# Kernel optimization log

Measured on AMD Instinct MI355X. Metric: run time of the kernel, lower is better.

## Reference

```python
import jax, jax.numpy as jnp
import numpy as np

N_NODE = 50000
N_EDGE = 800000
D = 64       # in_dim = out_dim = hidden_dim
A = 64       # attn_dim
N_REL = 475  # 2*237+1 relation ids
B = 32       # batch of queries


def setup_inputs() -> dict:
    key = jax.random.key(0)
    ks = jax.random.split(key, 16)
    hidden = jax.random.normal(ks[0], (N_NODE, D), dtype=jnp.float32)
    sub = jax.random.randint(ks[1], (N_EDGE,), 0, N_NODE)
    rel = jax.random.randint(ks[2], (N_EDGE,), 0, N_REL)
    obj = jax.random.randint(ks[3], (N_EDGE,), 0, N_NODE)
    edges = jnp.stack([sub, rel, obj], axis=1)  # [E, 3]
    gnn_emb_rel = jax.random.normal(ks[4], (N_REL, D), dtype=jnp.float32)
    mapping = jax.random.randint(ks[5], (N_REL,), 0, N_REL)  # rel id -> unique-rel row
    q_rel = jax.random.randint(ks[6], (B,), 0, N_REL)
    r_idx = jax.random.randint(ks[7], (N_EDGE,), 0, B)  # edge -> query index
    s = 1.0 / np.sqrt(D)
    sa = 1.0 / np.sqrt(A)
    u = lambda k, shape, b: jax.random.uniform(k, shape, jnp.float32, minval=-b, maxval=b)
    return {
        "hidden": hidden,
        "edges": edges,
        "gnn_emb_rel": gnn_emb_rel,
        "mapping": mapping,
        "q_rel": q_rel,
        "r_idx": r_idx,
        "n_node": N_NODE,
        "Ws_w": u(ks[8], (A, D), s),
        "Wr_w": u(ks[9], (A, D), s),
        "Wqr_w": u(ks[10], (A, D), s),
        "Wqr_b": u(ks[11], (A,), s),
        "walpha_w": u(ks[12], (1, A), sa),
        "walpha_b": u(ks[13], (1,), sa),
        "Wh_w": u(ks[14], (D, D), s),
    }


def reference(hidden, edges, gnn_emb_rel, mapping, q_rel, r_idx, n_node,
              Ws_w, Wr_w, Wqr_w, Wqr_b, walpha_w, walpha_b, Wh_w):
    sub, rel, obj = edges[:, 0], edges[:, 1], edges[:, 2]
    hs = hidden[sub]                       # [E, D] gather
    hr = gnn_emb_rel[mapping[rel]]         # [E, D] gather
    # per-query h_qr projected once, then gathered per edge (same math, cheaper)
    hq = gnn_emb_rel[mapping[q_rel]]       # [B, D]
    qr_attn = hq @ Wqr_w.T + Wqr_b         # [B, A]
    pre = hs @ Ws_w.T + hr @ Wr_w.T + qr_attn[r_idx]   # [E, A]
    alpha = jax.nn.sigmoid(jax.nn.relu(pre) @ walpha_w.T + walpha_b)  # [E, 1]
    message = alpha * (hs * hr)            # [E, D]
    message_agg = jax.ops.segment_sum(message, obj, num_segments=n_node)  # [N, D]
    hidden_new = jax.nn.relu(message_agg @ Wh_w.T)  # act = ReLU from GNN_auto
    return hidden_new
```

## Files before the change

kernel.cpp:

```cpp
#include <hip/hip_runtime.h>
#include <hip/hip_bf16.h>

#define D64 64
#define LPAD 68

typedef __attribute__((ext_vector_type(8))) short short8;
typedef __attribute__((ext_vector_type(4))) float f32x4;

__device__ inline float lane_bcast(float v, int l) {
    return __uint_as_float(__builtin_amdgcn_readlane(__float_as_uint(v), l));
}
__device__ inline float bf16_lo(unsigned u) { return __uint_as_float(u << 16); }
__device__ inline float bf16_hi(unsigned u) { return __uint_as_float(u & 0xFFFF0000u); }
__device__ inline float bf16u(unsigned short u) { return __uint_as_float((unsigned)u << 16); }
__device__ inline unsigned short f2bf(float f) {
    __hip_bfloat16 b = __float2bfloat16(f);
    return *(unsigned short*)&b;
}

__global__ void prep_kernel(const float* __restrict__ emb, const int* __restrict__ mapping,
                            const int* __restrict__ q_rel,
                            const float* __restrict__ Wr, const float* __restrict__ Wqr,
                            const float* __restrict__ Wqr_b, const float* __restrict__ Ws,
                            const float* __restrict__ Wh,
                            unsigned short* __restrict__ hrmapb,
                            unsigned short* __restrict__ hrWb,
                            unsigned short* __restrict__ qrb,
                            unsigned short* __restrict__ WsB,
                            unsigned short* __restrict__ WhB,
                            int* __restrict__ counts, int nrel, int nq, int NN) {
    int b = blockIdx.x;
    int lane = threadIdx.x;
    if (b < nrel) {
        int m = mapping[b];
        float v = emb[m * D64 + lane];
        hrmapb[b * D64 + lane] = f2bf(v);
        float acc = 0.f;
#pragma unroll
        for (int d = 0; d < D64; ++d)
            acc = fmaf(lane_bcast(v, d), Wr[lane * D64 + d], acc);
        hrWb[b * D64 + lane] = f2bf(acc);
    } else if (b < nrel + nq) {
        int q = b - nrel;
        int m = mapping[q_rel[q]];
        float v = emb[m * D64 + lane];
        float acc = Wqr_b[lane];
#pragma unroll
        for (int d = 0; d < D64; ++d)
            acc = fmaf(lane_bcast(v, d), Wqr[lane * D64 + d], acc);
        qrb[q * D64 + lane] = f2bf(acc);
    } else if (b < nrel + nq + 64) {
        int c = b - nrel - nq;
        WsB[c * D64 + lane] = f2bf(Ws[c * D64 + lane]);
    } else if (b < nrel + nq + 128) {
        int c = b - nrel - nq - 64;
        WhB[c * D64 + lane] = f2bf(Wh[c * D64 + lane]);
    } else {
        int c = b - nrel - nq - 128;
        int idx = c * 64 + lane;
        if (idx < NN) counts[idx] = 0;
    }
}

__global__ void comb_kernel(const unsigned short* __restrict__ hrWb,
                            const unsigned short* __restrict__ qrb,
                            unsigned short* __restrict__ combb, int nrel) {
    int i = blockIdx.x * blockDim.x + threadIdx.x;
    int total = nrel * 32 * D64;
    if (i < total) {
        int lane = i & 63;
        int row = i >> 6;
        int r = row >> 5;
        int q = row & 31;
        combb[i] = f2bf(bf16u(hrWb[r * D64 + lane]) + bf16u(qrb[q * D64 + lane]));
    }
}

__global__ void __launch_bounds__(64)
rowmm_mfma_kernel(const float* __restrict__ in,
                  const unsigned short* __restrict__ WsB,
                  unsigned short* __restrict__ outb,
                  unsigned short* __restrict__ inb, int nrows,
                  const int* __restrict__ edges, const int* __restrict__ r_idx,
                  int* __restrict__ counts, uint2* __restrict__ epack, int E) {
    __shared__ unsigned short la[16 * LPAD];
    int lane = threadIdx.x;
    int rbase = blockIdx.x * 16;

    if (rbase < nrows) {
        short8 bfrag[8];
#pragma unroll
        for (int t = 0; t < 4; ++t)
#pragma unroll
            for (int kk = 0; kk < 2; ++kk)
                bfrag[t * 2 + kk] = *(const short8*)(WsB + (size_t)(t * 16 + (lane & 15)) * D64 +
                                                     kk * 32 + (lane >> 4) * 8);

        bool full = (rbase + 16 <= nrows);
        float v[16];
        if (full) {
#pragma unroll
            for (int rr = 0; rr < 16; ++rr)
                v[rr] = in[(size_t)(rbase + rr) * D64 + lane];
        } else {
#pragma unroll
            for (int rr = 0; rr < 16; ++rr)
                v[rr] = (rbase + rr < nrows) ? in[(size_t)(rbase + rr) * D64 + lane] : 0.f;
        }
#pragma unroll
        for (int rr = 0; rr < 16; ++rr) {
            unsigned short bb = f2bf(v[rr]);
            if (rbase + rr < nrows) inb[(size_t)(rbase + rr) * D64 + lane] = bb;
            la[rr * LPAD + lane] = bb;
        }

        f32x4 acc[4];
#pragma unroll
        for (int t = 0; t < 4; ++t) acc[t] = (f32x4){0.f, 0.f, 0.f, 0.f};
#pragma unroll
        for (int kk = 0; kk < 2; ++kk) {
            short8 afrag = *(const short8*)(la + (lane & 15) * LPAD + kk * 32 + (lane >> 4) * 8);
#pragma unroll
            for (int t = 0; t < 4; ++t)
                acc[t] = __builtin_amdgcn_mfma_f32_16x16x32_bf16(afrag, bfrag[t * 2 + kk],
                                                                 acc[t], 0, 0, 0);
        }
#pragma unroll
        for (int t = 0; t < 4; ++t)
#pragma unroll
            for (int reg = 0; reg < 4; ++reg) {
                int row = rbase + (lane >> 4) * 4 + reg;
                int col = t * 16 + (lane & 15);
                if (row < nrows)
                    outb[(size_t)row * D64 + col] = f2bf(acc[t][reg]);
            }
    }

    int n4 = E >> 2;
    const uint4* e4 = (const uint4*)edges;
    for (int i4 = blockIdx.x * 64 + lane; i4 < n4; i4 += gridDim.x * 64) {
        uint4 a = e4[i4 * 3 + 0];
        uint4 b = e4[i4 * 3 + 1];
        uint4 c = e4[i4 * 3 + 2];
        uint4 r = ((const uint4*)r_idx)[i4];
        uint4 p01 = make_uint4(a.x | ((((a.y << 5) | r.x)) << 17), a.z,
                               a.w | ((((b.x << 5) | r.y)) << 17), b.y);
        uint4 p23 = make_uint4(b.z | ((((b.w << 5) | r.z)) << 17), c.x,
                               c.y | ((((c.z << 5) | r.w)) << 17), c.w);
        ((uint4*)epack)[i4 * 2 + 0] = p01;
        ((uint4*)epack)[i4 * 2 + 1] = p23;
        atomicAdd(&counts[a.z], 1);
        atomicAdd(&counts[b.y], 1);
        atomicAdd(&counts[c.x], 1);
        atomicAdd(&counts[c.w], 1);
    }
    int tail = n4 * 4;
    int gt = blockIdx.x * 64 + lane;
    int ti = tail + gt;
    if (gt < (E - tail) && ti < E) {
        unsigned sub = edges[ti * 3 + 0];
        unsigned rel = edges[ti * 3 + 1];
        unsigned obj = edges[ti * 3 + 2];
        unsigned ri  = r_idx[ti];
        epack[ti] = make_uint2(sub | (((rel << 5) | ri) << 17), obj);
        atomicAdd(&counts[obj], 1);
    }
}

__global__ void scan1_kernel(const int* __restrict__ counts, int* __restrict__ offs,
                             int* __restrict__ partials, int n) {
    __shared__ int tsum[256];
    int t = threadIdx.x;
    int base = blockIdx.x * 1024 + t * 4;
    int v[4];
    int s = 0;
#pragma unroll
    for (int i = 0; i < 4; ++i) {
        int idx = base + i;
        int c = (idx < n) ? counts[idx] : 0;
        v[i] = s;
        s += c;
    }
    tsum[t] = s;
    __syncthreads();
    for (int off = 1; off < 256; off <<= 1) {
        int y = (t >= off) ? tsum[t - off] : 0;
        __syncthreads();
        tsum[t] += y;
        __syncthreads();
    }
    int incl = tsum[t];
    int thread_prefix = incl - s;
    if (t == 255) partials[blockIdx.x] = incl;
#pragma unroll
    for (int i = 0; i < 4; ++i) {
        int idx = base + i;
        if (idx < n) offs[idx] = thread_prefix + v[i];
    }
}

__global__ void scan2_kernel(int* partials, int nb) {
    int t = threadIdx.x;
    int own = (t < nb) ? partials[t] : 0;
    int v = own;
    for (int off = 1; off < 64; off <<= 1) {
        int y = __shfl_up(v, off, 64);
        if (t >= off) v += y;
    }
    if (t < nb) partials[t] = v - own;
}

__global__ void scan3_kernel(int* __restrict__ offs, const int* __restrict__ partials, int n) {
    int base = blockIdx.x * 1024 + threadIdx.x;
    int add = partials[blockIdx.x];
#pragma unroll
    for (int i = 0; i < 4; ++i) {
        int idx = base + i * 256;
        if (idx < n) offs[idx] += add;
    }
}

__global__ void alpha_scatter_kernel(const uint2* __restrict__ epack,
                                     const unsigned short* __restrict__ hsWb,
                                     const unsigned short* __restrict__ combb,
                                     const float* __restrict__ walpha_w,
                                     const float* __restrict__ walpha_b,
                                     int* __restrict__ offs, int2* __restrict__ rec,
                                     int E, int half) {
    int tid = blockIdx.x * blockDim.x + threadIdx.x;
    int e0 = tid >> 3;
    int l = tid & 7;
    if (e0 >= half) return;
    int e1 = e0 + half;
    bool has1 = (e1 < E);

    uint2 p0 = epack[e0];
    uint2 p1 = has1 ? epack[e1] : make_uint2(0u, 0u);
    unsigned sub0 = p0.x & 0x1FFFF, comb0 = p0.x >> 17;
    unsigned sub1 = p1.x & 0x1FFFF, comb1 = p1.x >> 17;
    int obj0 = (int)p0.y, obj1 = (int)p1.y;

    uint4 hv0 = *(const uint4*)(hsWb  + (size_t)sub0  * D64 + l * 8);
    uint4 cv0 = *(const uint4*)(combb + (size_t)comb0 * D64 + l * 8);
    uint4 hv1 = *(const uint4*)(hsWb  + (size_t)sub1  * D64 + l * 8);
    uint4 cv1 = *(const uint4*)(combb + (size_t)comb1 * D64 + l * 8);
    const float4* w = (const float4*)(walpha_w + l * 8);
    float4 w0 = w[0], w1 = w[1];

    float x0, x1;
    x0 = fmaxf(bf16_lo(hv0.x) + bf16_lo(cv0.x), 0.f) * w0.x;
    x0 = fmaf(fmaxf(bf16_hi(hv0.x) + bf16_hi(cv0.x), 0.f), w0.y, x0);
    x0 = fmaf(fmaxf(bf16_lo(hv0.y) + bf16_lo(cv0.y), 0.f), w0.z, x0);
    x0 = fmaf(fmaxf(bf16_hi(hv0.y) + bf16_hi(cv0.y), 0.f), w0.w, x0);
    x0 = fmaf(fmaxf(bf16_lo(hv0.z) + bf16_lo(cv0.z), 0.f), w1.x, x0);
    x0 = fmaf(fmaxf(bf16_hi(hv0.z) + bf16_hi(cv0.z), 0.f), w1.y, x0);
    x0 = fmaf(fmaxf(bf16_lo(hv0.w) + bf16_lo(cv0.w), 0.f), w1.z, x0);
    x0 = fmaf(fmaxf(bf16_hi(hv0.w) + bf16_hi(cv0.w), 0.f), w1.w, x0);

    x1 = fmaxf(bf16_lo(hv1.x) + bf16_lo(cv1.x), 0.f) * w0.x;
    x1 = fmaf(fmaxf(bf16_hi(hv1.x) + bf16_hi(cv1.x), 0.f), w0.y, x1);
    x1 = fmaf(fmaxf(bf16_lo(hv1.y) + bf16_lo(cv1.y), 0.f), w0.z, x1);
    x1 = fmaf(fmaxf(bf16_hi(hv1.y) + bf16_hi(cv1.y), 0.f), w0.w, x1);
    x1 = fmaf(fmaxf(bf16_lo(hv1.z) + bf16_lo(cv1.z), 0.f), w1.x, x1);
    x1 = fmaf(fmaxf(bf16_hi(hv1.z) + bf16_hi(cv1.z), 0.f), w1.y, x1);
    x1 = fmaf(fmaxf(bf16_lo(hv1.w) + bf16_lo(cv1.w), 0.f), w1.z, x1);
    x1 = fmaf(fmaxf(bf16_hi(hv1.w) + bf16_hi(cv1.w), 0.f), w1.w, x1);

    x0 += __shfl_xor(x0, 4, 64);
    x1 += __shfl_xor(x1, 4, 64);
    x0 += __shfl_xor(x0, 2, 64);
    x1 += __shfl_xor(x1, 2, 64);
    x0 += __shfl_xor(x0, 1, 64);
    x1 += __shfl_xor(x1, 1, 64);

    if (l == 0) {
        float wb = walpha_b[0];
        float a0 = 1.f / (1.f + __expf(-(x0 + wb)));
        int rel0 = comb0 >> 5;
        int slot0 = atomicAdd(&offs[obj0], 1);
        rec[slot0] = make_int2((int)(sub0 | (rel0 << 17)), __float_as_int(a0));
        if (has1) {
            float a1 = 1.f / (1.f + __expf(-(x1 + wb)));
            int rel1 = comb1 >> 5;
            int slot1 = atomicAdd(&offs[obj1], 1);
            rec[slot1] = make_int2((int)(sub1 | (rel1 << 17)), __float_as_int(a1));
        }
    }
}

__global__ void agg_kernel(const int2* __restrict__ rec, const int* __restrict__ endoff,
                           const unsigned short* __restrict__ hiddenb,
                           const unsigned short* __restrict__ hrmapb,
                           unsigned short* __restrict__ aggb, int NN) {
    int tid = threadIdx.x;
    int lane = tid & 63;
    int n = (blockIdx.x * blockDim.x + tid) >> 6;
    if (n >= NN) return;
    int start = (n == 0) ? 0 : endoff[n - 1];
    int end = endoff[n];
    start = __builtin_amdgcn_readfirstlane(start);
    end = __builtin_amdgcn_readfirstlane(end);
    float acc0 = 0.f, acc1 = 0.f, acc2 = 0.f, acc3 = 0.f;
    for (int base = start; base < end; base += 64) {
        int cnt = end - base;
        if (cnt > 64) cnt = 64;
        int rx = 0, ry = 0;
        if (lane < cnt) {
            int2 r = rec[base + lane];
            rx = r.x; ry = r.y;
        }
        int j = 0;
        for (; j + 7 < cnt; j += 8) {
            int a_rx[8], a_ry[8];
#pragma unroll
            for (int k = 0; k < 8; ++k) {
                a_rx[k] = __builtin_amdgcn_readlane(rx, j + k);
                a_ry[k] = __builtin_amdgcn_readlane(ry, j + k);
            }
            float h[8], m[8];
#pragma unroll
            for (int k = 0; k < 8; ++k) {
                h[k] = bf16u(hiddenb[(size_t)(a_rx[k] & 0x1FFFF) * D64 + lane]);
                m[k] = bf16u(hrmapb[(size_t)((unsigned)a_rx[k] >> 17) * D64 + lane]);
            }
            acc0 = fmaf(__uint_as_float(a_ry[0]) * h[0], m[0], acc0);
            acc1 = fmaf(__uint_as_float(a_ry[1]) * h[1], m[1], acc1);
            acc2 = fmaf(__uint_as_float(a_ry[2]) * h[2], m[2], acc2);
            acc3 = fmaf(__uint_as_float(a_ry[3]) * h[3], m[3], acc3);
            acc0 = fmaf(__uint_as_float(a_ry[4]) * h[4], m[4], acc0);
            acc1 = fmaf(__uint_as_float(a_ry[5]) * h[5], m[5], acc1);
            acc2 = fmaf(__uint_as_float(a_ry[6]) * h[6], m[6], acc2);
            acc3 = fmaf(__uint_as_float(a_ry[7]) * h[7], m[7], acc3);
        }
        for (; j + 3 < cnt; j += 4) {
            int rx0 = __builtin_amdgcn_readlane(rx, j);
            int ry0 = __builtin_amdgcn_readlane(ry, j);
            int rx1 = __builtin_amdgcn_readlane(rx, j + 1);
            int ry1 = __builtin_amdgcn_readlane(ry, j + 1);
            int rx2 = __builtin_amdgcn_readlane(rx, j + 2);
            int ry2 = __builtin_amdgcn_readlane(ry, j + 2);
            int rx3 = __builtin_amdgcn_readlane(rx, j + 3);
            int ry3 = __builtin_amdgcn_readlane(ry, j + 3);
            float h0 = bf16u(hiddenb[(size_t)(rx0 & 0x1FFFF) * D64 + lane]);
            float m0 = bf16u(hrmapb[(size_t)((unsigned)rx0 >> 17) * D64 + lane]);
            float h1 = bf16u(hiddenb[(size_t)(rx1 & 0x1FFFF) * D64 + lane]);
            float m1 = bf16u(hrmapb[(size_t)((unsigned)rx1 >> 17) * D64 + lane]);
            float h2 = bf16u(hiddenb[(size_t)(rx2 & 0x1FFFF) * D64 + lane]);
            float m2 = bf16u(hrmapb[(size_t)((unsigned)rx2 >> 17) * D64 + lane]);
            float h3 = bf16u(hiddenb[(size_t)(rx3 & 0x1FFFF) * D64 + lane]);
            float m3 = bf16u(hrmapb[(size_t)((unsigned)rx3 >> 17) * D64 + lane]);
            acc0 = fmaf(__uint_as_float(ry0) * h0, m0, acc0);
            acc1 = fmaf(__uint_as_float(ry1) * h1, m1, acc1);
            acc2 = fmaf(__uint_as_float(ry2) * h2, m2, acc2);
            acc3 = fmaf(__uint_as_float(ry3) * h3, m3, acc3);
        }
        for (; j < cnt; ++j) {
            int rx0 = __builtin_amdgcn_readlane(rx, j);
            int ry0 = __builtin_amdgcn_readlane(ry, j);
            float h0 = bf16u(hiddenb[(size_t)(rx0 & 0x1FFFF) * D64 + lane]);
            float m0 = bf16u(hrmapb[(size_t)((unsigned)rx0 >> 17) * D64 + lane]);
            acc0 = fmaf(__uint_as_float(ry0) * h0, m0, acc0);
        }
    }
    aggb[(size_t)n * D64 + lane] = f2bf((acc0 + acc1) + (acc2 + acc3));
}

__global__ void rowmm_wh_kernel(const unsigned short* __restrict__ aggb,
                                const unsigned short* __restrict__ WhB,
                                float* __restrict__ out, int nrows) {
    int lane = threadIdx.x;
    int rbase = blockIdx.x * 16;
    if (rbase >= nrows) return;

    short8 bfrag[8];
#pragma unroll
    for (int t = 0; t < 4; ++t)
#pragma unroll
        for (int kk = 0; kk < 2; ++kk)
            bfrag[t * 2 + kk] = *(const short8*)(WhB + (size_t)(t * 16 + (lane & 15)) * D64 +
                                                 kk * 32 + (lane >> 4) * 8);

    f32x4 acc[4];
#pragma unroll
    for (int t = 0; t < 4; ++t) acc[t] = (f32x4){0.f, 0.f, 0.f, 0.f};
#pragma unroll
    for (int kk = 0; kk < 2; ++kk) {
        short8 afrag = *(const short8*)(aggb + (size_t)(rbase + (lane & 15)) * D64 +
                                        kk * 32 + (lane >> 4) * 8);
#pragma unroll
        for (int t = 0; t < 4; ++t)
            acc[t] = __builtin_amdgcn_mfma_f32_16x16x32_bf16(afrag, bfrag[t * 2 + kk],
                                                             acc[t], 0, 0, 0);
    }
#pragma unroll
    for (int t = 0; t < 4; ++t)
#pragma unroll
        for (int reg = 0; reg < 4; ++reg) {
            int row = rbase + (lane >> 4) * 4 + reg;
            int col = t * 16 + (lane & 15);
            if (row < nrows)
                out[(size_t)row * D64 + col] = fmaxf(acc[t][reg], 0.f);
        }
}

extern "C" void kernel_launch(void* const* d_in, const int* in_sizes, int n_in,
                              void* d_out, int out_size, void* d_ws, size_t ws_size,
                              hipStream_t stream) {
    const float* hidden   = (const float*)d_in[0];
    const int*   edges    = (const int*)d_in[1];
    const float* emb_rel  = (const float*)d_in[2];
    const int*   mapping  = (const int*)d_in[3];
    const int*   q_rel    = (const int*)d_in[4];
    const int*   r_idx    = (const int*)d_in[5];
    const float* Ws_w     = (const float*)d_in[7];
    const float* Wr_w     = (const float*)d_in[8];
    const float* Wqr_w    = (const float*)d_in[9];
    const float* Wqr_b    = (const float*)d_in[10];
    const float* walpha_w = (const float*)d_in[11];
    const float* walpha_b = (const float*)d_in[12];
    const float* Wh_w     = (const float*)d_in[13];
    float* out = (float*)d_out;

    int NN   = in_sizes[0] / D64;
    int E    = in_sizes[5];
    int NREL = in_sizes[3];
    int NQ   = in_sizes[4];

    char* ws = (char*)d_ws;
    size_t off = 0;
    unsigned short* hsWb    = (unsigned short*)(ws + off); off += (size_t)NN * D64 * 2;
    unsigned short* hiddenb = (unsigned short*)(ws + off); off += (size_t)NN * D64 * 2;
    int2*  rec  = (int2*)(ws + off);       off += (size_t)E * sizeof(int2);
    uint2* epack = (uint2*)(ws + off);     off += (size_t)E * sizeof(uint2);
    unsigned short* aggb = (unsigned short*)epack;
    int* counts = (int*)(ws + off);        off += (size_t)NN * sizeof(int);
    int* offs   = (int*)(ws + off);        off += (size_t)NN * sizeof(int);
    int* partials = (int*)(ws + off);      off += 64 * sizeof(int);
    unsigned short* hrmapb = (unsigned short*)(ws + off); off += (size_t)NREL * D64 * 2;
    unsigned short* hrWb   = (unsigned short*)(ws + off); off += (size_t)NREL * D64 * 2;
    unsigned short* qrb    = (unsigned short*)(ws + off); off += (size_t)NQ * D64 * 2;
    unsigned short* WsB    = (unsigned short*)(ws + off); off += (size_t)D64 * D64 * 2;
    unsigned short* WhB    = (unsigned short*)(ws + off); off += (size_t)D64 * D64 * 2;
    unsigned short* combb  = (unsigned short*)(ws + off); off += (size_t)NREL * 32 * D64 * 2;

    int NB = (NN + 1023) / 1024;
    int zblocks = (NN + 63) / 64;

    prep_kernel<<<NREL + NQ + 128 + zblocks, 64, 0, stream>>>(
        emb_rel, mapping, q_rel, Wr_w, Wqr_w, Wqr_b, Ws_w, Wh_w,
        hrmapb, hrWb, qrb, WsB, WhB, counts, NREL, NQ, NN);
    comb_kernel<<<(NREL * 32 * D64 + 255) / 256, 256, 0, stream>>>(hrWb, qrb, combb, NREL);
    rowmm_mfma_kernel<<<(NN + 15) / 16, 64, 0, stream>>>(hidden, WsB, hsWb, hiddenb, NN,
                                                         edges, r_idx, counts, epack, E);
    scan1_kernel<<<NB, 256, 0, stream>>>(counts, offs, partials, NN);
    scan2_kernel<<<1, 64, 0, stream>>>(partials, NB);
    scan3_kernel<<<NB, 256, 0, stream>>>(offs, partials, NN);
    {
        int half = (E + 1) / 2;
        long long threads = (long long)half * 8;
        int blocks = (int)((threads + 255) / 256);
        alpha_scatter_kernel<<<blocks, 256, 0, stream>>>(epack, hsWb, combb,
                                                         walpha_w, walpha_b, offs, rec, E, half);
    }
    agg_kernel<<<(NN * 64 + 1023) / 1024, 1024, 0, stream>>>(rec, offs, hiddenb, hrmapb,
                                                             aggb, NN);
    rowmm_wh_kernel<<<(NN + 15) / 16, 64, 0, stream>>>(aggb, WhB, out, NN);
}
```

Measured before the change: 139.8 us.

## Fuse attention computation into CSR aggregation and interleave projected/raw node features

Attention scoring moves out of the separate edge-parallel alpha_scatter kernel and into the per-node aggregation kernel, which recomputes alpha with a full 64-lane wave reduction for each edge. The projected features hs·Ws and the raw bf16 hidden values are stored interleaved as one 32-bit pair, so a single gather supplies both. The scatter step now writes a packed 4-byte record built straight from edges, which removes the intermediate epack buffer and the 8-byte alpha records. In exchange, aggregation does a 6-step shuffle reduction per edge and gathers from combb per lane, which adds serial work inside the node loop.

```diff
diff --git a/kernel.cpp b/kernel.cpp
--- a/kernel.cpp
+++ b/kernel.cpp
@@ -79,10 +79,9 @@
 __global__ void __launch_bounds__(64)
 rowmm_mfma_kernel(const float* __restrict__ in,
                   const unsigned short* __restrict__ WsB,
-                  unsigned short* __restrict__ outb,
-                  unsigned short* __restrict__ inb, int nrows,
-                  const int* __restrict__ edges, const int* __restrict__ r_idx,
-                  int* __restrict__ counts, uint2* __restrict__ epack, int E) {
+                  unsigned* __restrict__ pairb, int nrows,
+                  const int* __restrict__ edges,
+                  int* __restrict__ counts, int E) {
     __shared__ unsigned short la[16 * LPAD];
     int lane = threadIdx.x;
     int rbase = blockIdx.x * 16;
@@ -108,11 +107,8 @@
                 v[rr] = (rbase + rr < nrows) ? in[(size_t)(rbase + rr) * D64 + lane] : 0.f;
         }
 #pragma unroll
-        for (int rr = 0; rr < 16; ++rr) {
-            unsigned short bb = f2bf(v[rr]);
-            if (rbase + rr < nrows) inb[(size_t)(rbase + rr) * D64 + lane] = bb;
-            la[rr * LPAD + lane] = bb;
-        }
+        for (int rr = 0; rr < 16; ++rr)
+            la[rr * LPAD + lane] = f2bf(v[rr]);
 
         f32x4 acc[4];
 #pragma unroll
@@ -129,10 +125,14 @@
         for (int t = 0; t < 4; ++t)
 #pragma unroll
             for (int reg = 0; reg < 4; ++reg) {
-                int row = rbase + (lane >> 4) * 4 + reg;
+                int rl = (lane >> 4) * 4 + reg;
                 int col = t * 16 + (lane & 15);
-                if (row < nrows)
-                    outb[(size_t)row * D64 + col] = f2bf(acc[t][reg]);
+                int row = rbase + rl;
+                if (row < nrows) {
+                    unsigned hid = la[rl * LPAD + col];
+                    unsigned pr = (unsigned)f2bf(acc[t][reg]) | (hid << 16);
+                    pairb[(size_t)row * D64 + col] = pr;
+                }
             }
     }
 
@@ -142,13 +142,6 @@
         uint4 a = e4[i4 * 3 + 0];
         uint4 b = e4[i4 * 3 + 1];
         uint4 c = e4[i4 * 3 + 2];
-        uint4 r = ((const uint4*)r_idx)[i4];
-        uint4 p01 = make_uint4(a.x | ((((a.y << 5) | r.x)) << 17), a.z,
-                               a.w | ((((b.x << 5) | r.y)) << 17), b.y);
-        uint4 p23 = make_uint4(b.z | ((((b.w << 5) | r.z)) << 17), c.x,
-                               c.y | ((((c.z << 5) | r.w)) << 17), c.w);
-        ((uint4*)epack)[i4 * 2 + 0] = p01;
-        ((uint4*)epack)[i4 * 2 + 1] = p23;
         atomicAdd(&counts[a.z], 1);
         atomicAdd(&counts[b.y], 1);
         atomicAdd(&counts[c.x], 1);
@@ -157,14 +150,8 @@
     int tail = n4 * 4;
     int gt = blockIdx.x * 64 + lane;
     int ti = tail + gt;
-    if (gt < (E - tail) && ti < E) {
-        unsigned sub = edges[ti * 3 + 0];
-        unsigned rel = edges[ti * 3 + 1];
-        unsigned obj = edges[ti * 3 + 2];
-        unsigned ri  = r_idx[ti];
-        epack[ti] = make_uint2(sub | (((rel << 5) | ri) << 17), obj);
-        atomicAdd(&counts[obj], 1);
-    }
+    if (gt < (E - tail) && ti < E)
+        atomicAdd(&counts[edges[ti * 3 + 2]], 1);
 }
 
 __global__ void scan1_kernel(const int* __restrict__ counts, int* __restrict__ offs,
@@ -220,149 +207,109 @@
     }
 }
 
-__global__ void alpha_scatter_kernel(const uint2* __restrict__ epack,
-                                     const unsigned short* __restrict__ hsWb,
-                                     const unsigned short* __restrict__ combb,
-                                     const float* __restrict__ walpha_w,
-                                     const float* __restrict__ walpha_b,
-                                     int* __restrict__ offs, int2* __restrict__ rec,
-                                     int E, int half) {
-    int tid = blockIdx.x * blockDim.x + threadIdx.x;
-    int e0 = tid >> 3;
-    int l = tid & 7;
-    if (e0 >= half) return;
-    int e1 = e0 + half;
-    bool has1 = (e1 < E);
-
-    uint2 p0 = epack[e0];
-    uint2 p1 = has1 ? epack[e1] : make_uint2(0u, 0u);
-    unsigned sub0 = p0.x & 0x1FFFF, comb0 = p0.x >> 17;
-    unsigned sub1 = p1.x & 0x1FFFF, comb1 = p1.x >> 17;
-    int obj0 = (int)p0.y, obj1 = (int)p1.y;
-
-    uint4 hv0 = *(const uint4*)(hsWb  + (size_t)sub0  * D64 + l * 8);
-    uint4 cv0 = *(const uint4*)(combb + (size_t)comb0 * D64 + l * 8);
-    uint4 hv1 = *(const uint4*)(hsWb  + (size_t)sub1  * D64 + l * 8);
-    uint4 cv1 = *(const uint4*)(combb + (size_t)comb1 * D64 + l * 8);
-    const float4* w = (const float4*)(walpha_w + l * 8);
-    float4 w0 = w[0], w1 = w[1];
-
-    float x0, x1;
-    x0 = fmaxf(bf16_lo(hv0.x) + bf16_lo(cv0.x), 0.f) * w0.x;
-    x0 = fmaf(fmaxf(bf16_hi(hv0.x) + bf16_hi(cv0.x), 0.f), w0.y, x0);
-    x0 = fmaf(fmaxf(bf16_lo(hv0.y) + bf16_lo(cv0.y), 0.f), w0.z, x0);
-    x0 = fmaf(fmaxf(bf16_hi(hv0.y) + bf16_hi(cv0.y), 0.f), w0.w, x0);
-    x0 = fmaf(fmaxf(bf16_lo(hv0.z) + bf16_lo(cv0.z), 0.f), w1.x, x0);
-    x0 = fmaf(fmaxf(bf16_hi(hv0.z) + bf16_hi(cv0.z), 0.f), w1.y, x0);
-    x0 = fmaf(fmaxf(bf16_lo(hv0.w) + bf16_lo(cv0.w), 0.f), w1.z, x0);
-    x0 = fmaf(fmaxf(bf16_hi(hv0.w) + bf16_hi(cv0.w), 0.f), w1.w, x0);
-
-    x1 = fmaxf(bf16_lo(hv1.x) + bf16_lo(cv1.x), 0.f) * w0.x;
-    x1 = fmaf(fmaxf(bf16_hi(hv1.x) + bf16_hi(cv1.x), 0.f), w0.y, x1);
-    x1 = fmaf(fmaxf(bf16_lo(hv1.y) + bf16_lo(cv1.y), 0.f), w0.z, x1);
-    x1 = fmaf(fmaxf(bf16_hi(hv1.y) + bf16_hi(cv1.y), 0.f), w0.w, x1);
-    x1 = fmaf(fmaxf(bf16_lo(hv1.z) + bf16_lo(cv1.z), 0.f), w1.x, x1);
-    x1 = fmaf(fmaxf(bf16_hi(hv1.z) + bf16_hi(cv1.z), 0.f), w1.y, x1);
-    x1 = fmaf(fmaxf(bf16_lo(hv1.w) + bf16_lo(cv1.w), 0.f), w1.z, x1);
-    x1 = fmaf(fmaxf(bf16_hi(hv1.w) + bf16_hi(cv1.w), 0.f), w1.w, x1);
-
-    x0 += __shfl_xor(x0, 4, 64);
-    x1 += __shfl_xor(x1, 4, 64);
-    x0 += __shfl_xor(x0, 2, 64);
-    x1 += __shfl_xor(x1, 2, 64);
-    x0 += __shfl_xor(x0, 1, 64);
-    x1 += __shfl_xor(x1, 1, 64);
-
-    if (l == 0) {
-        float wb = walpha_b[0];
-        float a0 = 1.f / (1.f + __expf(-(x0 + wb)));
-        int rel0 = comb0 >> 5;
-        int slot0 = atomicAdd(&offs[obj0], 1);
-        rec[slot0] = make_int2((int)(sub0 | (rel0 << 17)), __float_as_int(a0));
-        if (has1) {
-            float a1 = 1.f / (1.f + __expf(-(x1 + wb)));
-            int rel1 = comb1 >> 5;
-            int slot1 = atomicAdd(&offs[obj1], 1);
-            rec[slot1] = make_int2((int)(sub1 | (rel1 << 17)), __float_as_int(a1));
-        }
-    }
-}
-
-__global__ void agg_kernel(const int2* __restrict__ rec, const int* __restrict__ endoff,
-                           const unsigned short* __restrict__ hiddenb,
+__global__ void scatter_kernel(const int* __restrict__ edges, const int* __restrict__ r_idx,
+                               int* __restrict__ offs, unsigned* __restrict__ rec, int E) {
+    int i4 = blockIdx.x * blockDim.x + threadIdx.x;
+    int n4 = E >> 2;
+    if (i4 < n4) {
+        const uint4* e4 = (const uint4*)edges;
+        uint4 a = e4[i4 * 3 + 0];
+        uint4 b = e4[i4 * 3 + 1];
+        uint4 c = e4[i4 * 3 + 2];
+        uint4 r = ((const uint4*)r_idx)[i4];
+        int s0 = atomicAdd(&offs[a.z], 1);
+        rec[s0] = a.x | ((((a.y << 5) | r.x)) << 17);
+        int s1 = atomicAdd(&offs[b.y], 1);
+        rec[s1] = a.w | ((((b.x << 5) | r.y)) << 17);
+        int s2 = atomicAdd(&offs[c.x], 1);
+        rec[s2] = b.z | ((((b.w << 5) | r.z)) << 17);
+        int s3 = atomicAdd(&offs[c.w], 1);
+        rec[s3] = c.y | ((((c.z << 5) | r.w)) << 17);
+    }
+    int tail = n4 * 4;
+    int ti = tail + i4;
+    if (i4 < (E - tail) && ti < E) {
+        unsigned sub = edges[ti * 3 + 0];
+        unsigned rel = edges[ti * 3 + 1];
+        unsigned obj = edges[ti * 3 + 2];
+        unsigned ri  = r_idx[ti];
+        int s = atomicAdd(&offs[(int)obj], 1);
+        rec[s] = sub | (((rel << 5) | ri) << 17);
+    }
+}
+
+__global__ void agg_kernel(const unsigned* __restrict__ rec, const int* __restrict__ endoff,
+                           const unsigned* __restrict__ pairb,
+                           const unsigned short* __restrict__ combb,
                            const unsigned short* __restrict__ hrmapb,
+                           const float* __restrict__ walpha_w,
+                           const float* __restrict__ walpha_b,
                            unsigned short* __restrict__ aggb, int NN) {
     int tid = threadIdx.x;
     int lane = tid & 63;
     int n = (blockIdx.x * blockDim.x + tid) >> 6;
     if (n >= NN) return;
+    float wa = walpha_w[lane];
+    float wb = walpha_b[0];
     int start = (n == 0) ? 0 : endoff[n - 1];
     int end = endoff[n];
     start = __builtin_amdgcn_readfirstlane(start);
     end = __builtin_amdgcn_readfirstlane(end);
-    float acc0 = 0.f, acc1 = 0.f, acc2 = 0.f, acc3 = 0.f;
+    float acc0 = 0.f, acc1 = 0.f;
     for (int base = start; base < end; base += 64) {
         int cnt = end - base;
         if (cnt > 64) cnt = 64;
-        int rx = 0, ry = 0;
-        if (lane < cnt) {
-            int2 r = rec[base + lane];
-            rx = r.x; ry = r.y;
+        unsigned rv = 0;
+        if (lane < cnt) rv = rec[base + lane];
+        int j = 0;
+        for (; j + 1 < cnt; j += 2) {
+            unsigned r0 = (unsigned)__builtin_amdgcn_readlane((int)rv, j);
+            unsigned r1 = (unsigned)__builtin_amdgcn_readlane((int)rv, j + 1);
+            unsigned sub0 = r0 & 0x1FFFF, cb0 = r0 >> 17;
+            unsigned sub1 = r1 & 0x1FFFF, cb1 = r1 >> 17;
+            unsigned pv0 = pairb[(size_t)sub0 * D64 + lane];
+            unsigned cv0 = (unsigned)combb[(size_t)cb0 * D64 + lane];
+            unsigned mv0 = (unsigned)hrmapb[(size_t)(cb0 >> 5) * D64 + lane];
+            unsigned pv1 = pairb[(size_t)sub1 * D64 + lane];
+            unsigned cv1 = (unsigned)combb[(size_t)cb1 * D64 + lane];
+            unsigned mv1 = (unsigned)hrmapb[(size_t)(cb1 >> 5) * D64 + lane];
+            float x0 = fmaxf(bf16_lo(pv0) + __uint_as_float(cv0 << 16), 0.f) * wa;
+            float x1 = fmaxf(bf16_lo(pv1) + __uint_as_float(cv1 << 16), 0.f) * wa;
+            x0 += __shfl_xor(x0, 32, 64);
+            x1 += __shfl_xor(x1, 32, 64);
+            x0 += __shfl_xor(x0, 16, 64);
+            x1 += __shfl_xor(x1, 16, 64);
+            x0 += __shfl_xor(x0, 8, 64);
+            x1 += __shfl_xor(x1, 8, 64);
+            x0 += __shfl_xor(x0, 4, 64);
+            x1 += __shfl_xor(x1, 4, 64);
+            x0 += __shfl_xor(x0, 2, 64);
+            x1 += __shfl_xor(x1, 2, 64);
+            x0 += __shfl_xor(x0, 1, 64);
+            x1 += __shfl_xor(x1, 1, 64);
+            float al0 = 1.f / (1.f + __expf(-(x0 + wb)));
+            float al1 = 1.f / (1.f + __expf(-(x1 + wb)));
+            acc0 = fmaf(al0 * bf16_hi(pv0), __uint_as_float(mv0 << 16), acc0);
+            acc1 = fmaf(al1 * bf16_hi(pv1), __uint_as_float(mv1 << 16), acc1);
         }
-        int j = 0;
-        for (; j + 7 < cnt; j += 8) {
-            int a_rx[8], a_ry[8];
-#pragma unroll
-            for (int k = 0; k < 8; ++k) {
-                a_rx[k] = __builtin_amdgcn_readlane(rx, j + k);
-                a_ry[k] = __builtin_amdgcn_readlane(ry, j + k);
-            }
-            float h[8], m[8];
-#pragma unroll
-            for (int k = 0; k < 8; ++k) {
-                h[k] = bf16u(hiddenb[(size_t)(a_rx[k] & 0x1FFFF) * D64 + lane]);
-                m[k] = bf16u(hrmapb[(size_t)((unsigned)a_rx[k] >> 17) * D64 + lane]);
-            }
-            acc0 = fmaf(__uint_as_float(a_ry[0]) * h[0], m[0], acc0);
-            acc1 = fmaf(__uint_as_float(a_ry[1]) * h[1], m[1], acc1);
-            acc2 = fmaf(__uint_as_float(a_ry[2]) * h[2], m[2], acc2);
-            acc3 = fmaf(__uint_as_float(a_ry[3]) * h[3], m[3], acc3);
-            acc0 = fmaf(__uint_as_float(a_ry[4]) * h[4], m[4], acc0);
-            acc1 = fmaf(__uint_as_float(a_ry[5]) * h[5], m[5], acc1);
-            acc2 = fmaf(__uint_as_float(a_ry[6]) * h[6], m[6], acc2);
-            acc3 = fmaf(__uint_as_float(a_ry[7]) * h[7], m[7], acc3);
+        if (j < cnt) {
+            unsigned r0 = (unsigned)__builtin_amdgcn_readlane((int)rv, j);
+            unsigned sub0 = r0 & 0x1FFFF, cb0 = r0 >> 17;
+            unsigned pv0 = pairb[(size_t)sub0 * D64 + lane];
+            unsigned cv0 = (unsigned)combb[(size_t)cb0 * D64 + lane];
+            unsigned mv0 = (unsigned)hrmapb[(size_t)(cb0 >> 5) * D64 + lane];
+            float x0 = fmaxf(bf16_lo(pv0) + __uint_as_float(cv0 << 16), 0.f) * wa;
+            x0 += __shfl_xor(x0, 32, 64);
+            x0 += __shfl_xor(x0, 16, 64);
+            x0 += __shfl_xor(x0, 8, 64);
+            x0 += __shfl_xor(x0, 4, 64);
+            x0 += __shfl_xor(x0, 2, 64);
+            x0 += __shfl_xor(x0, 1, 64);
+            float al0 = 1.f / (1.f + __expf(-(x0 + wb)));
+            acc0 = fmaf(al0 * bf16_hi(pv0), __uint_as_float(mv0 << 16), acc0);
         }
-        for (; j + 3 < cnt; j += 4) {
-            int rx0 = __builtin_amdgcn_readlane(rx, j);
-            int ry0 = __builtin_amdgcn_readlane(ry, j);
-            int rx1 = __builtin_amdgcn_readlane(rx, j + 1);
-            int ry1 = __builtin_amdgcn_readlane(ry, j + 1);
-            int rx2 = __builtin_amdgcn_readlane(rx, j + 2);
-            int ry2 = __builtin_amdgcn_readlane(ry, j + 2);
-            int rx3 = __builtin_amdgcn_readlane(rx, j + 3);
-            int ry3 = __builtin_amdgcn_readlane(ry, j + 3);
-            float h0 = bf16u(hiddenb[(size_t)(rx0 & 0x1FFFF) * D64 + lane]);
-            float m0 = bf16u(hrmapb[(size_t)((unsigned)rx0 >> 17) * D64 + lane]);
-            float h1 = bf16u(hiddenb[(size_t)(rx1 & 0x1FFFF) * D64 + lane]);
-            float m1 = bf16u(hrmapb[(size_t)((unsigned)rx1 >> 17) * D64 + lane]);
-            float h2 = bf16u(hiddenb[(size_t)(rx2 & 0x1FFFF) * D64 + lane]);
-            float m2 = bf16u(hrmapb[(size_t)((unsigned)rx2 >> 17) * D64 + lane]);
-            float h3 = bf16u(hiddenb[(size_t)(rx3 & 0x1FFFF) * D64 + lane]);
-            float m3 = bf16u(hrmapb[(size_t)((unsigned)rx3 >> 17) * D64 + lane]);
-            acc0 = fmaf(__uint_as_float(ry0) * h0, m0, acc0);
-            acc1 = fmaf(__uint_as_float(ry1) * h1, m1, acc1);
-            acc2 = fmaf(__uint_as_float(ry2) * h2, m2, acc2);
-            acc3 = fmaf(__uint_as_float(ry3) * h3, m3, acc3);
-        }
-        for (; j < cnt; ++j) {
-            int rx0 = __builtin_amdgcn_readlane(rx, j);
-            int ry0 = __builtin_amdgcn_readlane(ry, j);
-            float h0 = bf16u(hiddenb[(size_t)(rx0 & 0x1FFFF) * D64 + lane]);
-            float m0 = bf16u(hrmapb[(size_t)((unsigned)rx0 >> 17) * D64 + lane]);
-            acc0 = fmaf(__uint_as_float(ry0) * h0, m0, acc0);
-        }
-    }
-    aggb[(size_t)n * D64 + lane] = f2bf((acc0 + acc1) + (acc2 + acc3));
+    }
+    aggb[(size_t)n * D64 + lane] = f2bf(acc0 + acc1);
 }
 
 __global__ void rowmm_wh_kernel(const unsigned short* __restrict__ aggb,
@@ -428,11 +375,9 @@
 
     char* ws = (char*)d_ws;
     size_t off = 0;
-    unsigned short* hsWb    = (unsigned short*)(ws + off); off += (size_t)NN * D64 * 2;
-    unsigned short* hiddenb = (unsigned short*)(ws + off); off += (size_t)NN * D64 * 2;
-    int2*  rec  = (int2*)(ws + off);       off += (size_t)E * sizeof(int2);
-    uint2* epack = (uint2*)(ws + off);     off += (size_t)E * sizeof(uint2);
-    unsigned short* aggb = (unsigned short*)epack;
+    unsigned* pairb  = (unsigned*)(ws + off);       off += (size_t)NN * D64 * 4;
+    unsigned short* aggb = (unsigned short*)(ws + off); off += (size_t)NN * D64 * 2;
+    unsigned* rec    = (unsigned*)(ws + off);       off += (size_t)E * 4;
     int* counts = (int*)(ws + off);        off += (size_t)NN * sizeof(int);
     int* offs   = (int*)(ws + off);        off += (size_t)NN * sizeof(int);
     int* partials = (int*)(ws + off);      off += 64 * sizeof(int);
@@ -450,19 +395,16 @@
         emb_rel, mapping, q_rel, Wr_w, Wqr_w, Wqr_b, Ws_w, Wh_w,
         hrmapb, hrWb, qrb, WsB, WhB, counts, NREL, NQ, NN);
     comb_kernel<<<(NREL * 32 * D64 + 255) / 256, 256, 0, stream>>>(hrWb, qrb, combb, NREL);
-    rowmm_mfma_kernel<<<(NN + 15) / 16, 64, 0, stream>>>(hidden, WsB, hsWb, hiddenb, NN,
-                                                         edges, r_idx, counts, epack, E);
+    rowmm_mfma_kernel<<<(NN + 15) / 16, 64, 0, stream>>>(hidden, WsB, pairb, NN,
+                                                         edges, counts, E);
     scan1_kernel<<<NB, 256, 0, stream>>>(counts, offs, partials, NN);
     scan2_kernel<<<1, 64, 0, stream>>>(partials, NB);
     scan3_kernel<<<NB, 256, 0, stream>>>(offs, partials, NN);
     {
-        int half = (E + 1) / 2;
-        long long threads = (long long)half * 8;
-        int blocks = (int)((threads + 255) / 256);
-        alpha_scatter_kernel<<<blocks, 256, 0, stream>>>(epack, hsWb, combb,
-                                                         walpha_w, walpha_b, offs, rec, E, half);
-    }
-    agg_kernel<<<(NN * 64 + 1023) / 1024, 1024, 0, stream>>>(rec, offs, hiddenb, hrmapb,
-                                                             aggb, NN);
+        int n4 = (E + 3) / 4;
+        scatter_kernel<<<(n4 + 255) / 256, 256, 0, stream>>>(edges, r_idx, offs, rec, E);
+    }
+    agg_kernel<<<(NN * 64 + 1023) / 1024, 1024, 0, stream>>>(rec, offs, pairb, combb, hrmapb,
+                                                             walpha_w, walpha_b, aggb, NN);
     rowmm_wh_kernel<<<(NN + 15) / 16, 64, 0, stream>>>(aggb, WhB, out, NN);
 }
```

Result: slower. 195.3 us (+39.7%).
